# Kernel optimization log

Hardware: AMD Instinct MI355X
Metric: run time of the kernel (lower is better)

Reference implementation:

```python
import jax, jax.numpy as jnp
import numpy as np

B, K, N, E, T = 4096, 64, 100000, 128, 3


def setup_inputs() -> dict:
    key = jax.random.key(0)
    ks = jax.random.split(key, 16)
    f = lambda i, shape: jax.random.normal(ks[i], shape, dtype=jnp.float32) * 0.05
    return dict(
        nodes=jax.random.randint(ks[0], (B,), 0, N),
        neigh_idx=jax.random.randint(ks[1], (T, B, K), 0, N),
        node_emb=f(2, (N, E)),
        node_prof=f(3, (N, E)),
        neigh_emb=f(4, (T, N, E)),
        neigh_prof=f(5, (T, N, E)),
        W_f=f(6, (2 * E, E)), b_f=jnp.zeros((E,), jnp.float32),
        Wa1=f(7, (2 * E, E)), ba1=jnp.zeros((E,), jnp.float32),
        Wa2=f(8, (E, E)), ba2=jnp.zeros((E,), jnp.float32),
        Wa3=f(9, (E, 1)), ba3=jnp.zeros((1,), jnp.float32),
        W1=f(10, (E, E)), b1=jnp.zeros((E,), jnp.float32),
        W2=f(11, (E, E)), b2=jnp.zeros((E,), jnp.float32),
        Wc=f(12, (2 * E, E)), bc=jnp.zeros((E,), jnp.float32),
        Wt=f(13, (T * E, T)),
    )


def reference(nodes, neigh_idx, node_emb, node_prof, neigh_emb, neigh_prof,
              W_f, b_f, Wa1, ba1, Wa2, ba2, Wa3, ba3,
              W1, b1, W2, b2, Wc, bc, Wt):
    # fusion(emb, profile) = relu(Linear(concat(emb, profile)))
    fuse = lambda e, p: jax.nn.relu(jnp.concatenate([e, p], -1) @ W_f + b_f)

    nodes_fusion = fuse(node_emb[nodes], node_prof[nodes])            # [B,E]

    per_type = []
    for t in range(T):                                                 # small fixed loop over types
        idx = neigh_idx[t]                                             # [B,K]
        nf = fuse(neigh_emb[t][idx], neigh_prof[t][idx])               # [B,K,E]
        # attention MLP over (neighbor, node) pairs -> softmax over K neighbors
        x = jnp.concatenate(
            [nf, jnp.broadcast_to(nodes_fusion[:, None, :], nf.shape)], -1)  # [B,K,2E]
        h = jax.nn.relu(x @ Wa1 + ba1)
        h = jax.nn.relu(h @ Wa2 + ba2)
        att = jax.nn.softmax((h @ Wa3 + ba3).squeeze(-1), axis=1)      # [B,K]
        agg = jnp.einsum('bke,bk->be', nf, att)                        # weighted neighbor sum
        per_type.append(jax.nn.relu(agg @ W1 + b1))                    # linear_1 + relu

    type_agg = jnp.concatenate(per_type, axis=1)                       # [B,T*E]
    att_t = jax.nn.softmax(type_agg @ Wt, axis=1)                      # [B,T]
    final = jnp.einsum('bte,bt->be', type_agg.reshape(B, T, E), att_t)
    final = jax.nn.relu(final @ W2 + b2)                               # linear_2 + relu
    out = jax.nn.relu(jnp.concatenate([nodes_fusion, final], 1) @ Wc + bc)
    return out, att_t[:, :, None]
```

## Files before the change

### kernel.cpp

```cpp
#include <hip/hip_runtime.h>
#include <hip/hip_bf16.h>

#define B_ 4096
#define K_ 64
#define N_ 100000
#define E_ 128
#define T_ 3

typedef __bf16 bf16x8 __attribute__((ext_vector_type(8)));
typedef float  f32x4  __attribute__((ext_vector_type(4)));

static __device__ __forceinline__ bf16x8 cvt8r(f32x4 u, f32x4 v) {
    bf16x8 o;
    o[0] = (__bf16)u[0]; o[1] = (__bf16)u[1]; o[2] = (__bf16)u[2]; o[3] = (__bf16)u[3];
    o[4] = (__bf16)v[0]; o[5] = (__bf16)v[1]; o[6] = (__bf16)v[2]; o[7] = (__bf16)v[3];
    return o;
}

typedef const __attribute__((address_space(1))) void GAS;
typedef __attribute__((address_space(3))) void LAS;
static __device__ __forceinline__ void gload16(const void* g, void* l) {
    __builtin_amdgcn_global_load_lds((GAS*)g, (LAS*)l, 16, 0, 0);
}

#define MFMA16(a, b, c) __builtin_amdgcn_mfma_f32_16x16x32_bf16((a), (b), (c), 0, 0, 0)

__global__ __launch_bounds__(256)
void k_prep(const float* __restrict__ W_f, const float* __restrict__ Wa1,
            const float* __restrict__ Wa2, const float* __restrict__ W1,
            __bf16* __restrict__ WtF, __bf16* __restrict__ Wa1t,
            __bf16* __restrict__ Wa2t, __bf16* __restrict__ W1t) {
    const int n = blockIdx.x;
    const int k = threadIdx.x;
    if (blockIdx.y == 0) {
        WtF[n * 256 + k] = (__bf16)W_f[k * 128 + n];
    } else if (blockIdx.y == 1) {
        if (k < 128) Wa1t[n * 128 + k] = (__bf16)Wa1[k * 128 + n];
    } else if (blockIdx.y == 2) {
        if (k < 128) Wa2t[n * 128 + k] = (__bf16)Wa2[k * 128 + n];
    } else {
        if (k < 128) W1t[n * 128 + k] = (__bf16)W1[k * 128 + n];
    }
}

__global__ __launch_bounds__(128)
void k_node_fusion(const int* __restrict__ nodes,
                   const float* __restrict__ node_emb,
                   const float* __restrict__ node_prof,
                   const float* __restrict__ W_f, const float* __restrict__ b_f,
                   __bf16* __restrict__ nodes_fusion) {
    __shared__ float x[256];
    const int b = blockIdx.x;
    const int e = threadIdx.x;
    const int nd = nodes[b];
    x[e]       = node_emb[(size_t)nd * E_ + e];
    x[128 + e] = node_prof[(size_t)nd * E_ + e];
    __syncthreads();
    float acc = b_f[e];
#pragma unroll 8
    for (int i = 0; i < 256; ++i) acc = fmaf(x[i], W_f[i * E_ + e], acc);
    nodes_fusion[(size_t)b * E_ + e] = (__bf16)fmaxf(acc, 0.f);
}

__global__ __launch_bounds__(128)
void k_node_pre(const __bf16* __restrict__ nodes_fusion,
                const float* __restrict__ Wa1, const float* __restrict__ ba1,
                float* __restrict__ node_pre) {
    __shared__ float x[128];
    const int b = blockIdx.x;
    const int c = threadIdx.x;
    x[c] = (float)nodes_fusion[(size_t)b * E_ + c];
    __syncthreads();
    float acc = ba1[c];
#pragma unroll 8
    for (int i = 0; i < 128; ++i) acc = fmaf(x[i], Wa1[(128 + i) * E_ + c], acc);
    node_pre[(size_t)b * E_ + c] = acc;
}

#define NF_GRID 512
#define NF_TPT (N_ / 32)
#define NF_NJOB (NF_TPT * T_)

__global__ __launch_bounds__(256, 2)
void k_nf(const float* __restrict__ neigh_emb,
          const float* __restrict__ neigh_prof,
          const __bf16* __restrict__ WtF, const float* __restrict__ b_f,
          const __bf16* __restrict__ Wa1t, const __bf16* __restrict__ W1t,
          __bf16* __restrict__ G, __bf16* __restrict__ M1) {
    __shared__ __align__(16) float  Xf[2][32 * 256];
    __shared__ __align__(16) __bf16 NFl[32 * 128];

    const int tid  = threadIdx.x;
    const int wid  = tid >> 6, lane = tid & 63;
    const int lr   = lane & 15, lk = lane >> 4;

    bf16x8 wf[16];
#pragma unroll
    for (int ks = 0; ks < 8; ++ks)
#pragma unroll
        for (int n = 0; n < 2; ++n)
            wf[ks * 2 + n] = *(const bf16x8*)&WtF[
                (size_t)(wid * 32 + n * 16 + lr) * 256 + ks * 32 + lk * 8];
    bf16x8 wa[8], w1r[8];
#pragma unroll
    for (int ks = 0; ks < 4; ++ks)
#pragma unroll
        for (int n = 0; n < 2; ++n) {
            wa[ks * 2 + n]  = *(const bf16x8*)&Wa1t[
                (size_t)(wid * 32 + n * 16 + lr) * 128 + ks * 32 + lk * 8];
            w1r[ks * 2 + n] = *(const bf16x8*)&W1t[
                (size_t)(wid * 32 + n * 16 + lr) * 128 + ks * 32 + lk * 8];
        }
    const float bb0 = b_f[wid * 32 + lr];
    const float bb1 = b_f[wid * 32 + 16 + lr];

    auto stage = [&](int j, int buf) {
        const int t    = j / NF_TPT;
        const int base = (j - t * NF_TPT) * 32;
        const float* embT  = neigh_emb  + (size_t)t * N_ * E_;
        const float* profT = neigh_prof + (size_t)t * N_ * E_;
#pragma unroll
        for (int i = 0; i < 8; ++i) {
            const int r  = wid * 8 + i;
            const int id = base + r;
            const int g  = lane ^ (r & 15);
            const float* src = (g < 32)
                ? embT  + (size_t)id * E_ + g * 4
                : profT + (size_t)id * E_ + (g - 32) * 4;
            gload16(src, (char*)&Xf[buf][0] + r * 1024);
        }
    };

    int job = blockIdx.x;
    stage(job, 0);
    int cur = 0;
    bool first = true;

    for (; job < NF_NJOB; job += NF_GRID) {
        const int tc    = job / NF_TPT;
        const int basec = (job - tc * NF_TPT) * 32;

        if (first) { asm volatile("s_waitcnt vmcnt(0)" ::: "memory"); first = false; }
        else       { asm volatile("s_waitcnt vmcnt(4)" ::: "memory"); }
        __builtin_amdgcn_s_barrier();
        __builtin_amdgcn_sched_barrier(0);

        const int nxt = job + NF_GRID;
        if (nxt < NF_NJOB) stage(nxt, cur ^ 1);

        const float* X = &Xf[cur][0];

        {
            f32x4 acc1[2][2] = {};
#pragma unroll
            for (int ks = 0; ks < 8; ++ks) {
                const int g0 = ks * 8 + lk * 2;
                const f32x4 u0 = *(const f32x4*)&X[lr * 256 + ((g0 ^ lr) << 2)];
                const f32x4 v0 = *(const f32x4*)&X[lr * 256 + (((g0 + 1) ^ lr) << 2)];
                const f32x4 u1 = *(const f32x4*)&X[(16 + lr) * 256 + ((g0 ^ lr) << 2)];
                const f32x4 v1 = *(const f32x4*)&X[(16 + lr) * 256 + (((g0 + 1) ^ lr) << 2)];
                const bf16x8 a0 = cvt8r(u0, v0);
                const bf16x8 a1 = cvt8r(u1, v1);
                acc1[0][0] = MFMA16(a0, wf[ks * 2 + 0], acc1[0][0]);
                acc1[0][1] = MFMA16(a0, wf[ks * 2 + 1], acc1[0][1]);
                acc1[1][0] = MFMA16(a1, wf[ks * 2 + 0], acc1[1][0]);
                acc1[1][1] = MFMA16(a1, wf[ks * 2 + 1], acc1[1][1]);
            }
#pragma unroll
            for (int n = 0; n < 2; ++n) {
                const int c = wid * 32 + n * 16 + lr;
                const float bb = n ? bb1 : bb0;
                const int q = c >> 3, eo = c & 7;
#pragma unroll
                for (int mi = 0; mi < 2; ++mi)
#pragma unroll
                    for (int j = 0; j < 4; ++j) {
                        const int rN = mi * 16 + lk * 4 + j;
                        NFl[rN * 128 + ((q ^ (rN & 15)) << 3) + eo] =
                            (__bf16)fmaxf(acc1[mi][n][j] + bb, 0.f);
                    }
            }
        }
        asm volatile("s_waitcnt lgkmcnt(0)" ::: "memory");
        __builtin_amdgcn_s_barrier();
        __builtin_amdgcn_sched_barrier(0);

        {
            f32x4 g2[2][2] = {}, g3[2][2] = {};
#pragma unroll
            for (int ks = 0; ks < 4; ++ks) {
                const int q = ks * 4 + lk;
                const bf16x8 a0 = *(const bf16x8*)&NFl[lr * 128 + ((q ^ lr) << 3)];
                const bf16x8 a1 = *(const bf16x8*)&NFl[(16 + lr) * 128 + ((q ^ lr) << 3)];
#pragma unroll
                for (int n = 0; n < 2; ++n) {
                    g2[0][n] = MFMA16(a0, wa[ks * 2 + n],  g2[0][n]);
                    g2[1][n] = MFMA16(a1, wa[ks * 2 + n],  g2[1][n]);
                    g3[0][n] = MFMA16(a0, w1r[ks * 2 + n], g3[0][n]);
                    g3[1][n] = MFMA16(a1, w1r[ks * 2 + n], g3[1][n]);
                }
            }
            __bf16* Gl  = (__bf16*)&Xf[cur][0];
            __bf16* M1l = Gl + 4096;
#pragma unroll
            for (int n = 0; n < 2; ++n) {
                const int c = wid * 32 + n * 16 + lr;
                const int q = c >> 3, eo = c & 7;
#pragma unroll
                for (int mi = 0; mi < 2; ++mi)
#pragma unroll
                    for (int j = 0; j < 4; ++j) {
                        const int rN = mi * 16 + lk * 4 + j;
                        const int sl = rN * 128 + ((q ^ (rN & 15)) << 3) + eo;
                        Gl[sl]  = (__bf16)g2[mi][n][j];
                        M1l[sl] = (__bf16)g3[mi][n][j];
                    }
            }
        }
        asm volatile("s_waitcnt lgkmcnt(0)" ::: "memory");
        __builtin_amdgcn_s_barrier();
        __builtin_amdgcn_sched_barrier(0);

        {
            const __bf16* Gl  = (const __bf16*)&Xf[cur][0];
            const __bf16* M1l = Gl + 4096;
            const int rr = tid >> 3, qq = tid & 7;
            __bf16* gout = G  + ((size_t)tc * N_ + basec + rr) * E_;
            __bf16* mout = M1 + ((size_t)tc * N_ + basec + rr) * E_;
#pragma unroll
            for (int g = 0; g < 2; ++g) {
                const int q = qq * 2 + g;
                const int p = q ^ (rr & 15);
                *(bf16x8*)(gout + q * 8) = *(const bf16x8*)&Gl[rr * 128 + (p << 3)];
                *(bf16x8*)(mout + q * 8) = *(const bf16x8*)&M1l[rr * 128 + (p << 3)];
            }
        }
        cur ^= 1;
    }
}

__global__ __launch_bounds__(256, 4)
void k_att(const int* __restrict__ neigh_idx,
           const __bf16* __restrict__ G, const __bf16* __restrict__ M1,
           const __bf16* __restrict__ Wa2t,
           const float* __restrict__ ba2,
           const float* __restrict__ Wa3, const float* __restrict__ ba3,
           const float* __restrict__ node_pre,
           const float* __restrict__ b1,
           __bf16* __restrict__ type_agg) {
    __shared__ __align__(16) __bf16 Gb[64 * 128];
    __shared__ __align__(16) __bf16 Mb[64 * 128];
    __shared__ float npre[128];
    __shared__ float scp[128];
    __shared__ float att_s[64];
    __shared__ float red2[2][128];

    const int b   = blockIdx.x;
    const int t   = blockIdx.y;
    const int tid = threadIdx.x;
    const int wid = tid >> 6, lane = tid & 63;
    const int lr = lane & 15, lk = lane >> 4;

    if (tid < 128) npre[tid] = node_pre[(size_t)b * E_ + tid];

    const int* idx_row = neigh_idx + ((size_t)t * B_ + b) * K_;

#pragma unroll
    for (int i = 0; i < 4; ++i) {
        const int rowblock = wid * 16 + i * 4;
        const int row = rowblock + (lane >> 4);
        const int q = (lane & 15) ^ (row & 15);
        const int id = idx_row[row];
        const size_t goff = ((size_t)t * N_ + id) * E_ + q * 8;
        gload16(G + goff,  (char*)Gb + rowblock * 256);
        gload16(M1 + goff, (char*)Mb + rowblock * 256);
    }
    __syncthreads();

    const int mp = wid >> 1, h = wid & 1;
    const int r0 = 32 * mp + lr, r1 = r0 + 16;
    f32x4 acc[2][4] = {};
#pragma unroll
    for (int ks = 0; ks < 4; ++ks) {
        const int q = ks * 4 + lk;
        const f32x4 n0 = *(const f32x4*)&npre[q * 8];
        const f32x4 n1 = *(const f32x4*)&npre[q * 8 + 4];
        const bf16x8 g0 = *(const bf16x8*)&Gb[r0 * 128 + ((q ^ lr) << 3)];
        const bf16x8 g1 = *(const bf16x8*)&Gb[r1 * 128 + ((q ^ lr) << 3)];
        bf16x8 a0, a1;
#pragma unroll
        for (int j = 0; j < 4; ++j) {
            a0[j]     = (__bf16)fmaxf((float)g0[j]     + n0[j], 0.f);
            a0[j + 4] = (__bf16)fmaxf((float)g0[j + 4] + n1[j], 0.f);
            a1[j]     = (__bf16)fmaxf((float)g1[j]     + n0[j], 0.f);
            a1[j + 4] = (__bf16)fmaxf((float)g1[j + 4] + n1[j], 0.f);
        }
        const __bf16* wb = Wa2t + (size_t)(h * 64 + lr) * 128 + ks * 32 + lk * 8;
#pragma unroll
        for (int n = 0; n < 4; ++n) {
            const bf16x8 w = *(const bf16x8*)(wb + (size_t)n * 16 * 128);
            acc[0][n] = MFMA16(a0, w, acc[0][n]);
            acc[1][n] = MFMA16(a1, w, acc[1][n]);
        }
    }

    {
        float ba2r[4], wa3r[4];
#pragma unroll
        for (int n = 0; n < 4; ++n) {
            const int col = h * 64 + n * 16 + lr;
            ba2r[n] = ba2[col];
            wa3r[n] = Wa3[col];
        }
#pragma unroll
        for (int mi = 0; mi < 2; ++mi)
#pragma unroll
            for (int j = 0; j < 4; ++j) {
                float v = 0.f;
#pragma unroll
                for (int n = 0; n < 4; ++n)
                    v += fmaxf(acc[mi][n][j] + ba2r[n], 0.f) * wa3r[n];
                v += __shfl_xor(v, 1);
                v += __shfl_xor(v, 2);
                v += __shfl_xor(v, 4);
                v += __shfl_xor(v, 8);
                if (lr == 0)
                    scp[h * 64 + 32 * mp + mi * 16 + lk * 4 + j] = v;
            }
    }
    __syncthreads();

    if (tid < 64) {
        const float v = scp[tid] + scp[64 + tid] + ba3[0];
        float m = v;
#pragma unroll
        for (int o = 32; o > 0; o >>= 1) m = fmaxf(m, __shfl_xor(m, o));
        const float pe = __expf(v - m);
        float s = pe;
#pragma unroll
        for (int o = 32; o > 0; o >>= 1) s += __shfl_xor(s, o);
        att_s[tid] = pe / s;
    }
    __syncthreads();

    {
        const int e = tid & 127, half = tid >> 7;
        const int q = e >> 3, eo = e & 7;
        float a = 0.f;
#pragma unroll 8
        for (int n = 0; n < 32; ++n) {
            const int nn = half * 32 + n;
            a = fmaf(att_s[nn], (float)Mb[nn * 128 + ((q ^ (nn & 15)) << 3) + eo], a);
        }
        red2[half][e] = a;
    }
    __syncthreads();
    if (tid < 128) {
        const float s = red2[0][tid] + red2[1][tid];
        type_agg[((size_t)b * T_ + t) * E_ + tid] = (__bf16)fmaxf(s + b1[tid], 0.f);
    }
}

__global__ __launch_bounds__(128)
void k_final(const __bf16* __restrict__ type_agg,
             const __bf16* __restrict__ nodes_fusion,
             const float* __restrict__ Wt,
             const float* __restrict__ W2, const float* __restrict__ b2,
             const float* __restrict__ Wc, const float* __restrict__ bc,
             float* __restrict__ out, float* __restrict__ att_out) {
    __shared__ float ta[384];
    __shared__ float nfu[128];
    __shared__ float fin[128];
    __shared__ float hb[128];
    __shared__ float att[3];
    __shared__ float red[3][128];

    const int b = blockIdx.x;
    const int e = threadIdx.x;

    const float v0 = (float)type_agg[(size_t)b * 384 + e];
    const float v1 = (float)type_agg[(size_t)b * 384 + 128 + e];
    const float v2 = (float)type_agg[(size_t)b * 384 + 256 + e];
    ta[e] = v0; ta[128 + e] = v1; ta[256 + e] = v2;
    nfu[e] = (float)nodes_fusion[(size_t)b * E_ + e];

    float p0, p1, p2;
    {
        const float* w0 = Wt + (size_t)e * 3;
        const float* w1 = Wt + (size_t)(128 + e) * 3;
        const float* w2 = Wt + (size_t)(256 + e) * 3;
        p0 = v0 * w0[0] + v1 * w1[0] + v2 * w2[0];
        p1 = v0 * w0[1] + v1 * w1[1] + v2 * w2[1];
        p2 = v0 * w0[2] + v1 * w1[2] + v2 * w2[2];
    }
    red[0][e] = p0; red[1][e] = p1; red[2][e] = p2;
    __syncthreads();

    if (e < 3) {
        float s = 0.f;
        for (int i = 0; i < 128; ++i) s += red[e][i];
        red[e][0] = s;
    }
    __syncthreads();
    if (e == 0) {
        const float s0 = red[0][0], s1 = red[1][0], s2 = red[2][0];
        const float m  = fmaxf(s0, fmaxf(s1, s2));
        const float e0 = __expf(s0 - m), e1 = __expf(s1 - m), e2 = __expf(s2 - m);
        const float inv = 1.f / (e0 + e1 + e2);
        att[0] = e0 * inv; att[1] = e1 * inv; att[2] = e2 * inv;
    }
    __syncthreads();

    fin[e] = att[0] * ta[e] + att[1] * ta[128 + e] + att[2] * ta[256 + e];
    __syncthreads();

    float acc = b2[e];
#pragma unroll 8
    for (int i = 0; i < 128; ++i) acc = fmaf(fin[i], W2[i * E_ + e], acc);
    hb[e] = fmaxf(acc, 0.f);
    __syncthreads();

    float acc2 = bc[e];
#pragma unroll 8
    for (int i = 0; i < 128; ++i) acc2 = fmaf(nfu[i], Wc[i * E_ + e], acc2);
#pragma unroll 8
    for (int i = 0; i < 128; ++i) acc2 = fmaf(hb[i], Wc[(128 + i) * E_ + e], acc2);
    out[(size_t)b * E_ + e] = fmaxf(acc2, 0.f);

    if (e < 3) att_out[(size_t)b * 3 + e] = att[e];
}

extern "C" void kernel_launch(void* const* d_in, const int* in_sizes, int n_in,
                              void* d_out, int out_size, void* d_ws, size_t ws_size,
                              hipStream_t stream) {
    const int*   nodes      = (const int*)d_in[0];
    const int*   neigh_idx  = (const int*)d_in[1];
    const float* node_emb   = (const float*)d_in[2];
    const float* node_prof  = (const float*)d_in[3];
    const float* neigh_emb  = (const float*)d_in[4];
    const float* neigh_prof = (const float*)d_in[5];
    const float* W_f = (const float*)d_in[6];  const float* b_f = (const float*)d_in[7];
    const float* Wa1 = (const float*)d_in[8];  const float* ba1 = (const float*)d_in[9];
    const float* Wa2 = (const float*)d_in[10]; const float* ba2 = (const float*)d_in[11];
    const float* Wa3 = (const float*)d_in[12]; const float* ba3 = (const float*)d_in[13];
    const float* W1  = (const float*)d_in[14]; const float* b1  = (const float*)d_in[15];
    const float* W2  = (const float*)d_in[16]; const float* b2  = (const float*)d_in[17];
    const float* Wc  = (const float*)d_in[18]; const float* bc  = (const float*)d_in[19];
    const float* Wt  = (const float*)d_in[20];

    float* out     = (float*)d_out;
    float* att_out = out + (size_t)B_ * E_;

    char* ws = (char*)d_ws;
    __bf16* nodes_fusion = (__bf16*)(ws);
    float*  node_pre     = (float*)(ws + (1u << 20));
    __bf16* type_agg     = (__bf16*)(ws + (3u << 20));
    __bf16* WtF          = (__bf16*)(ws + (6u << 20));
    __bf16* Wa1t         = (__bf16*)(ws + (6u << 20) + 65536);
    __bf16* Wa2t         = (__bf16*)(ws + (6u << 20) + 98304);
    __bf16* W1t          = (__bf16*)(ws + (6u << 20) + 131072);
    __bf16* Gt           = (__bf16*)(ws + (8u << 20));
    __bf16* M1t          = (__bf16*)(ws + (88u << 20));

    k_prep<<<dim3(128, 4), 256, 0, stream>>>(W_f, Wa1, Wa2, W1, WtF, Wa1t, Wa2t, W1t);
    k_node_fusion<<<B_, 128, 0, stream>>>(nodes, node_emb, node_prof, W_f, b_f,
                                          nodes_fusion);
    k_node_pre<<<B_, 128, 0, stream>>>(nodes_fusion, Wa1, ba1, node_pre);
    k_nf<<<NF_GRID, 256, 0, stream>>>(neigh_emb, neigh_prof,
                                      WtF, b_f, Wa1t, W1t, Gt, M1t);
    k_att<<<dim3(B_, T_), 256, 0, stream>>>(neigh_idx, Gt, M1t, Wa2t, ba2,
                                            Wa3, ba3, node_pre, b1, type_agg);
    k_final<<<B_, 128, 0, stream>>>(type_agg, nodes_fusion, Wt, W2, b2, Wc, bc,
                                    out, att_out);
}
```

Baseline: 281.2 us.

## Store only neighbor fusion; move Wa1 into attention and W1 after aggregation

Result: slower. 315.2 us (+12.1%).

```diff
diff --git a/kernel.cpp b/kernel.cpp
--- a/kernel.cpp
+++ b/kernel.cpp
@@ -77,18 +77,17 @@
     node_pre[(size_t)b * E_ + c] = acc;
 }
 
-#define NF_GRID 512
-#define NF_TPT (N_ / 32)
+#define NF_GRID 1024
+#define NF_TPT (N_ / 16)
 #define NF_NJOB (NF_TPT * T_)
 
-__global__ __launch_bounds__(256, 2)
+__global__ __launch_bounds__(256, 4)
 void k_nf(const float* __restrict__ neigh_emb,
           const float* __restrict__ neigh_prof,
           const __bf16* __restrict__ WtF, const float* __restrict__ b_f,
-          const __bf16* __restrict__ Wa1t, const __bf16* __restrict__ W1t,
-          __bf16* __restrict__ G, __bf16* __restrict__ M1) {
-    __shared__ __align__(16) float  Xf[2][32 * 256];
-    __shared__ __align__(16) __bf16 NFl[32 * 128];
+          __bf16* __restrict__ NFt) {
+    __shared__ __align__(16) float  Xf[2][16 * 256];
+    __shared__ __align__(16) __bf16 NFl[16 * 128];
 
     const int tid  = threadIdx.x;
     const int wid  = tid >> 6, lane = tid & 63;
@@ -101,27 +100,17 @@
         for (int n = 0; n < 2; ++n)
             wf[ks * 2 + n] = *(const bf16x8*)&WtF[
                 (size_t)(wid * 32 + n * 16 + lr) * 256 + ks * 32 + lk * 8];
-    bf16x8 wa[8], w1r[8];
-#pragma unroll
-    for (int ks = 0; ks < 4; ++ks)
-#pragma unroll
-        for (int n = 0; n < 2; ++n) {
-            wa[ks * 2 + n]  = *(const bf16x8*)&Wa1t[
-                (size_t)(wid * 32 + n * 16 + lr) * 128 + ks * 32 + lk * 8];
-            w1r[ks * 2 + n] = *(const bf16x8*)&W1t[
-                (size_t)(wid * 32 + n * 16 + lr) * 128 + ks * 32 + lk * 8];
-        }
     const float bb0 = b_f[wid * 32 + lr];
     const float bb1 = b_f[wid * 32 + 16 + lr];
 
     auto stage = [&](int j, int buf) {
         const int t    = j / NF_TPT;
-        const int base = (j - t * NF_TPT) * 32;
+        const int base = (j - t * NF_TPT) * 16;
         const float* embT  = neigh_emb  + (size_t)t * N_ * E_;
         const float* profT = neigh_prof + (size_t)t * N_ * E_;
 #pragma unroll
-        for (int i = 0; i < 8; ++i) {
-            const int r  = wid * 8 + i;
+        for (int i = 0; i < 4; ++i) {
+            const int r  = wid * 4 + i;
             const int id = base + r;
             const int g  = lane ^ (r & 15);
             const float* src = (g < 32)
@@ -138,10 +127,10 @@
 
     for (; job < NF_NJOB; job += NF_GRID) {
         const int tc    = job / NF_TPT;
-        const int basec = (job - tc * NF_TPT) * 32;
+        const int basec = (job - tc * NF_TPT) * 16;
 
         if (first) { asm volatile("s_waitcnt vmcnt(0)" ::: "memory"); first = false; }
-        else       { asm volatile("s_waitcnt vmcnt(4)" ::: "memory"); }
+        else       { asm volatile("s_waitcnt vmcnt(1)" ::: "memory"); }
         __builtin_amdgcn_s_barrier();
         __builtin_amdgcn_sched_barrier(0);
 
@@ -151,20 +140,15 @@
         const float* X = &Xf[cur][0];
 
         {
-            f32x4 acc1[2][2] = {};
+            f32x4 acc1[2] = {};
 #pragma unroll
             for (int ks = 0; ks < 8; ++ks) {
                 const int g0 = ks * 8 + lk * 2;
                 const f32x4 u0 = *(const f32x4*)&X[lr * 256 + ((g0 ^ lr) << 2)];
                 const f32x4 v0 = *(const f32x4*)&X[lr * 256 + (((g0 + 1) ^ lr) << 2)];
-                const f32x4 u1 = *(const f32x4*)&X[(16 + lr) * 256 + ((g0 ^ lr) << 2)];
-                const f32x4 v1 = *(const f32x4*)&X[(16 + lr) * 256 + (((g0 + 1) ^ lr) << 2)];
                 const bf16x8 a0 = cvt8r(u0, v0);
-                const bf16x8 a1 = cvt8r(u1, v1);
-                acc1[0][0] = MFMA16(a0, wf[ks * 2 + 0], acc1[0][0]);
-                acc1[0][1] = MFMA16(a0, wf[ks * 2 + 1], acc1[0][1]);
-                acc1[1][0] = MFMA16(a1, wf[ks * 2 + 0], acc1[1][0]);
-                acc1[1][1] = MFMA16(a1, wf[ks * 2 + 1], acc1[1][1]);
+                acc1[0] = MFMA16(a0, wf[ks * 2 + 0], acc1[0]);
+                acc1[1] = MFMA16(a0, wf[ks * 2 + 1], acc1[1]);
             }
 #pragma unroll
             for (int n = 0; n < 2; ++n) {
@@ -172,13 +156,11 @@
                 const float bb = n ? bb1 : bb0;
                 const int q = c >> 3, eo = c & 7;
 #pragma unroll
-                for (int mi = 0; mi < 2; ++mi)
-#pragma unroll
-                    for (int j = 0; j < 4; ++j) {
-                        const int rN = mi * 16 + lk * 4 + j;
-                        NFl[rN * 128 + ((q ^ (rN & 15)) << 3) + eo] =
-                            (__bf16)fmaxf(acc1[mi][n][j] + bb, 0.f);
-                    }
+                for (int j = 0; j < 4; ++j) {
+                    const int rN = lk * 4 + j;
+                    NFl[rN * 128 + ((q ^ rN) << 3) + eo] =
+                        (__bf16)fmaxf(acc1[n][j] + bb, 0.f);
+                }
             }
         }
         asm volatile("s_waitcnt lgkmcnt(0)" ::: "memory");
@@ -186,54 +168,10 @@
         __builtin_amdgcn_sched_barrier(0);
 
         {
-            f32x4 g2[2][2] = {}, g3[2][2] = {};
-#pragma unroll
-            for (int ks = 0; ks < 4; ++ks) {
-                const int q = ks * 4 + lk;
-                const bf16x8 a0 = *(const bf16x8*)&NFl[lr * 128 + ((q ^ lr) << 3)];
-                const bf16x8 a1 = *(const bf16x8*)&NFl[(16 + lr) * 128 + ((q ^ lr) << 3)];
-#pragma unroll
-                for (int n = 0; n < 2; ++n) {
-                    g2[0][n] = MFMA16(a0, wa[ks * 2 + n],  g2[0][n]);
-                    g2[1][n] = MFMA16(a1, wa[ks * 2 + n],  g2[1][n]);
-                    g3[0][n] = MFMA16(a0, w1r[ks * 2 + n], g3[0][n]);
-                    g3[1][n] = MFMA16(a1, w1r[ks * 2 + n], g3[1][n]);
-                }
-            }
-            __bf16* Gl  = (__bf16*)&Xf[cur][0];
-            __bf16* M1l = Gl + 4096;
-#pragma unroll
-            for (int n = 0; n < 2; ++n) {
-                const int c = wid * 32 + n * 16 + lr;
-                const int q = c >> 3, eo = c & 7;
-#pragma unroll
-                for (int mi = 0; mi < 2; ++mi)
-#pragma unroll
-                    for (int j = 0; j < 4; ++j) {
-                        const int rN = mi * 16 + lk * 4 + j;
-                        const int sl = rN * 128 + ((q ^ (rN & 15)) << 3) + eo;
-                        Gl[sl]  = (__bf16)g2[mi][n][j];
-                        M1l[sl] = (__bf16)g3[mi][n][j];
-                    }
-            }
-        }
-        asm volatile("s_waitcnt lgkmcnt(0)" ::: "memory");
-        __builtin_amdgcn_s_barrier();
-        __builtin_amdgcn_sched_barrier(0);
-
-        {
-            const __bf16* Gl  = (const __bf16*)&Xf[cur][0];
-            const __bf16* M1l = Gl + 4096;
-            const int rr = tid >> 3, qq = tid & 7;
-            __bf16* gout = G  + ((size_t)tc * N_ + basec + rr) * E_;
-            __bf16* mout = M1 + ((size_t)tc * N_ + basec + rr) * E_;
-#pragma unroll
-            for (int g = 0; g < 2; ++g) {
-                const int q = qq * 2 + g;
-                const int p = q ^ (rr & 15);
-                *(bf16x8*)(gout + q * 8) = *(const bf16x8*)&Gl[rr * 128 + (p << 3)];
-                *(bf16x8*)(mout + q * 8) = *(const bf16x8*)&M1l[rr * 128 + (p << 3)];
-            }
+            const int rr = tid >> 4, qq = tid & 15;
+            const int p = qq ^ (rr & 15);
+            __bf16* outp = NFt + ((size_t)tc * N_ + basec + rr) * E_ + qq * 8;
+            *(bf16x8*)outp = *(const bf16x8*)&NFl[rr * 128 + (p << 3)];
         }
         cur ^= 1;
     }
@@ -241,15 +179,15 @@
 
 __global__ __launch_bounds__(256, 4)
 void k_att(const int* __restrict__ neigh_idx,
-           const __bf16* __restrict__ G, const __bf16* __restrict__ M1,
+           const __bf16* __restrict__ NFt,
+           const __bf16* __restrict__ Wa1t,
            const __bf16* __restrict__ Wa2t,
            const float* __restrict__ ba2,
            const float* __restrict__ Wa3, const float* __restrict__ ba3,
            const float* __restrict__ node_pre,
-           const float* __restrict__ b1,
-           __bf16* __restrict__ type_agg) {
-    __shared__ __align__(16) __bf16 Gb[64 * 128];
-    __shared__ __align__(16) __bf16 Mb[64 * 128];
+           __bf16* __restrict__ aggB) {
+    __shared__ __align__(16) __bf16 Nb[64 * 128];
+    __shared__ __align__(16) __bf16 H1l[64 * 128];
     __shared__ float npre[128];
     __shared__ float scp[128];
     __shared__ float att_s[64];
@@ -271,40 +209,63 @@
         const int row = rowblock + (lane >> 4);
         const int q = (lane & 15) ^ (row & 15);
         const int id = idx_row[row];
-        const size_t goff = ((size_t)t * N_ + id) * E_ + q * 8;
-        gload16(G + goff,  (char*)Gb + rowblock * 256);
-        gload16(M1 + goff, (char*)Mb + rowblock * 256);
+        gload16(NFt + ((size_t)t * N_ + id) * E_ + q * 8,
+                (char*)Nb + rowblock * 256);
+    }
+    __syncthreads();
+
+    {
+        f32x4 acc2[4][2] = {};
+#pragma unroll
+        for (int ks = 0; ks < 4; ++ks) {
+            const int q = ks * 4 + lk;
+            bf16x8 a[4];
+#pragma unroll
+            for (int mi = 0; mi < 4; ++mi)
+                a[mi] = *(const bf16x8*)&Nb[(mi * 16 + lr) * 128 + ((q ^ lr) << 3)];
+#pragma unroll
+            for (int n = 0; n < 2; ++n) {
+                const bf16x8 w = *(const bf16x8*)&Wa1t[
+                    (size_t)(wid * 32 + n * 16 + lr) * 128 + ks * 32 + lk * 8];
+#pragma unroll
+                for (int mi = 0; mi < 4; ++mi)
+                    acc2[mi][n] = MFMA16(a[mi], w, acc2[mi][n]);
+            }
+        }
+#pragma unroll
+        for (int n = 0; n < 2; ++n) {
+            const int col = wid * 32 + n * 16 + lr;
+            const float pp = npre[col];
+            const int q = col >> 3, eo = col & 7;
+#pragma unroll
+            for (int mi = 0; mi < 4; ++mi)
+#pragma unroll
+                for (int j = 0; j < 4; ++j) {
+                    const int row = mi * 16 + lk * 4 + j;
+                    H1l[row * 128 + ((q ^ (row & 15)) << 3) + eo] =
+                        (__bf16)fmaxf(acc2[mi][n][j] + pp, 0.f);
+                }
+        }
     }
     __syncthreads();
 
     const int mp = wid >> 1, h = wid & 1;
     const int r0 = 32 * mp + lr, r1 = r0 + 16;
-    f32x4 acc[2][4] = {};
-#pragma unroll
-    for (int ks = 0; ks < 4; ++ks) {
-        const int q = ks * 4 + lk;
-        const f32x4 n0 = *(const f32x4*)&npre[q * 8];
-        const f32x4 n1 = *(const f32x4*)&npre[q * 8 + 4];
-        const bf16x8 g0 = *(const bf16x8*)&Gb[r0 * 128 + ((q ^ lr) << 3)];
-        const bf16x8 g1 = *(const bf16x8*)&Gb[r1 * 128 + ((q ^ lr) << 3)];
-        bf16x8 a0, a1;
-#pragma unroll
-        for (int j = 0; j < 4; ++j) {
-            a0[j]     = (__bf16)fmaxf((float)g0[j]     + n0[j], 0.f);
-            a0[j + 4] = (__bf16)fmaxf((float)g0[j + 4] + n1[j], 0.f);
-            a1[j]     = (__bf16)fmaxf((float)g1[j]     + n0[j], 0.f);
-            a1[j + 4] = (__bf16)fmaxf((float)g1[j + 4] + n1[j], 0.f);
-        }
-        const __bf16* wb = Wa2t + (size_t)(h * 64 + lr) * 128 + ks * 32 + lk * 8;
-#pragma unroll
-        for (int n = 0; n < 4; ++n) {
-            const bf16x8 w = *(const bf16x8*)(wb + (size_t)n * 16 * 128);
-            acc[0][n] = MFMA16(a0, w, acc[0][n]);
-            acc[1][n] = MFMA16(a1, w, acc[1][n]);
-        }
-    }
-
     {
+        f32x4 acc[2][4] = {};
+#pragma unroll
+        for (int ks = 0; ks < 4; ++ks) {
+            const int q = ks * 4 + lk;
+            const bf16x8 a0 = *(const bf16x8*)&H1l[r0 * 128 + ((q ^ lr) << 3)];
+            const bf16x8 a1 = *(const bf16x8*)&H1l[r1 * 128 + ((q ^ lr) << 3)];
+            const __bf16* wb = Wa2t + (size_t)(h * 64 + lr) * 128 + ks * 32 + lk * 8;
+#pragma unroll
+            for (int n = 0; n < 4; ++n) {
+                const bf16x8 w = *(const bf16x8*)(wb + (size_t)n * 16 * 128);
+                acc[0][n] = MFMA16(a0, w, acc[0][n]);
+                acc[1][n] = MFMA16(a1, w, acc[1][n]);
+            }
+        }
         float ba2r[4], wa3r[4];
 #pragma unroll
         for (int n = 0; n < 4; ++n) {
@@ -350,14 +311,46 @@
 #pragma unroll 8
         for (int n = 0; n < 32; ++n) {
             const int nn = half * 32 + n;
-            a = fmaf(att_s[nn], (float)Mb[nn * 128 + ((q ^ (nn & 15)) << 3) + eo], a);
+            a = fmaf(att_s[nn], (float)Nb[nn * 128 + ((q ^ (nn & 15)) << 3) + eo], a);
         }
         red2[half][e] = a;
     }
     __syncthreads();
     if (tid < 128) {
-        const float s = red2[0][tid] + red2[1][tid];
-        type_agg[((size_t)b * T_ + t) * E_ + tid] = (__bf16)fmaxf(s + b1[tid], 0.f);
+        aggB[((size_t)b * T_ + t) * E_ + tid] = (__bf16)(red2[0][tid] + red2[1][tid]);
+    }
+}
+
+__global__ __launch_bounds__(256)
+void k_w1(const __bf16* __restrict__ aggB, const __bf16* __restrict__ W1t,
+          const float* __restrict__ b1, __bf16* __restrict__ type_agg) {
+    const int tid  = threadIdx.x;
+    const int wid  = tid >> 6;
+    const int lane = tid & 63;
+    const int lr   = lane & 15;
+    const int lk   = lane >> 4;
+    const int rbase = blockIdx.x * 64 + wid * 16;
+
+    f32x4 acc[8] = {};
+#pragma unroll
+    for (int ks = 0; ks < 4; ++ks) {
+        const bf16x8 a = *(const bf16x8*)&aggB[(size_t)(rbase + lr) * 128 + ks * 32 + lk * 8];
+        const __bf16* wb = W1t + (size_t)lr * 128 + ks * 32 + lk * 8;
+#pragma unroll
+        for (int n = 0; n < 8; ++n) {
+            const bf16x8 w = *(const bf16x8*)(wb + (size_t)n * 16 * 128);
+            acc[n] = MFMA16(a, w, acc[n]);
+        }
+    }
+#pragma unroll
+    for (int n = 0; n < 8; ++n) {
+        const int col = n * 16 + lr;
+        const float bb = b1[col];
+#pragma unroll
+        for (int j = 0; j < 4; ++j) {
+            const int row = rbase + lk * 4 + j;
+            type_agg[(size_t)row * 128 + col] = (__bf16)fmaxf(acc[n][j] + bb, 0.f);
+        }
     }
 }
 
@@ -455,21 +448,21 @@
     __bf16* nodes_fusion = (__bf16*)(ws);
     float*  node_pre     = (float*)(ws + (1u << 20));
     __bf16* type_agg     = (__bf16*)(ws + (3u << 20));
-    __bf16* WtF          = (__bf16*)(ws + (6u << 20));
-    __bf16* Wa1t         = (__bf16*)(ws + (6u << 20) + 65536);
-    __bf16* Wa2t         = (__bf16*)(ws + (6u << 20) + 98304);
-    __bf16* W1t          = (__bf16*)(ws + (6u << 20) + 131072);
-    __bf16* Gt           = (__bf16*)(ws + (8u << 20));
-    __bf16* M1t          = (__bf16*)(ws + (88u << 20));
+    __bf16* aggB         = (__bf16*)(ws + (6u << 20));
+    __bf16* WtF          = (__bf16*)(ws + (9u << 20));
+    __bf16* Wa1t         = (__bf16*)(ws + (9u << 20) + 65536);
+    __bf16* Wa2t         = (__bf16*)(ws + (9u << 20) + 98304);
+    __bf16* W1t          = (__bf16*)(ws + (9u << 20) + 131072);
+    __bf16* NFt          = (__bf16*)(ws + (16u << 20));
 
     k_prep<<<dim3(128, 4), 256, 0, stream>>>(W_f, Wa1, Wa2, W1, WtF, Wa1t, Wa2t, W1t);
     k_node_fusion<<<B_, 128, 0, stream>>>(nodes, node_emb, node_prof, W_f, b_f,
                                           nodes_fusion);
     k_node_pre<<<B_, 128, 0, stream>>>(nodes_fusion, Wa1, ba1, node_pre);
-    k_nf<<<NF_GRID, 256, 0, stream>>>(neigh_emb, neigh_prof,
-                                      WtF, b_f, Wa1t, W1t, Gt, M1t);
-    k_att<<<dim3(B_, T_), 256, 0, stream>>>(neigh_idx, Gt, M1t, Wa2t, ba2,
-                                            Wa3, ba3, node_pre, b1, type_agg);
+    k_nf<<<NF_GRID, 256, 0, stream>>>(neigh_emb, neigh_prof, WtF, b_f, NFt);
+    k_att<<<dim3(B_, T_), 256, 0, stream>>>(neigh_idx, NFt, Wa1t, Wa2t, ba2,
+                                            Wa3, ba3, node_pre, aggB);
+    k_w1<<<(B_ * T_) / 64, 256, 0, stream>>>(aggB, W1t, b1, type_agg);
     k_final<<<B_, 128, 0, stream>>>(type_agg, nodes_fusion, Wt, W2, b2, Wc, bc,
                                     out, att_out);
 }
```
